# Kernel optimization log

Hardware: AMD Instinct MI355X
Metric: run time of the kernel (lower is better)

## Reference

```python
import jax, jax.numpy as jnp
import numpy as np

CODE_DIM = 256
CODEBOOK_SIZE = 8192
N = 32768
BETA = 0.25


def setup_inputs() -> dict:
    key = jax.random.key(0)
    k1, k2 = jax.random.split(key)
    z = jax.random.normal(k1, (N, CODE_DIM), dtype=jnp.float32)
    # nn.Embedding weight init: uniform(-1/code_dim, 1/code_dim)
    codebook = jax.random.uniform(
        k2, (CODEBOOK_SIZE, CODE_DIM), dtype=jnp.float32,
        minval=-1.0 / CODE_DIM, maxval=1.0 / CODE_DIM)
    return {"z": z, "codebook": codebook}


def reference(z, codebook):
    # z: (N, D) already flat (z.view(N, -1) in torch). codebook: (K, D)
    # squared euclidean distances via expansion: ||z||^2 - 2 z.E^T + ||E||^2
    z_sq = jnp.sum(z * z, axis=1, keepdims=True)            # (N, 1)
    e_sq = jnp.sum(codebook * codebook, axis=1)             # (K,)
    dist = z_sq - 2.0 * (z @ codebook.T) + e_sq[None, :]    # (N, K)
    indices = jnp.argmin(dist, axis=1)                      # (N,)
    z_q = codebook[indices]                                 # (N, D)

    commitment_loss = jnp.mean((jax.lax.stop_gradient(z_q) - z) ** 2)
    codebook_loss = jnp.mean((z_q - jax.lax.stop_gradient(z)) ** 2)
    loss = BETA * commitment_loss + codebook_loss

    # straight-through estimator
    z_q_ste = z + jax.lax.stop_gradient(z_q - z)
    return (z_q_ste, loss)
```

## Files before the change

### kernel.cpp

```cpp
#include <hip/hip_runtime.h>
#include <cfloat>

#define NROWS  32768
#define NCODES 8192
#define DDIM   256
#define KG     4
#define CPB    (NCODES / KG)
#define CT     64
#define TPB    (CPB / CT)
#define RPB    256

typedef __attribute__((ext_vector_type(8))) __bf16 bf16x8;
typedef __attribute__((ext_vector_type(4))) float  f32x4;

__global__ __launch_bounds__(256)
void cvt_cb(const float* __restrict__ cb, __bf16* __restrict__ cbb,
            float* __restrict__ esq) {
    const size_t i = (size_t)(blockIdx.x * 256 + threadIdx.x) * 8;
    const float4 f0 = *(const float4*)(cb + i);
    const float4 f1 = *(const float4*)(cb + i + 4);
    bf16x8 v;
    v[0] = (__bf16)f0.x; v[1] = (__bf16)f0.y; v[2] = (__bf16)f0.z; v[3] = (__bf16)f0.w;
    v[4] = (__bf16)f1.x; v[5] = (__bf16)f1.y; v[6] = (__bf16)f1.z; v[7] = (__bf16)f1.w;
    *(bf16x8*)(cbb + i) = v;
    float s = f0.x * f0.x + f0.y * f0.y + f0.z * f0.z + f0.w * f0.w
            + f1.x * f1.x + f1.y * f1.y + f1.z * f1.z + f1.w * f1.w;
    for (int o = 16; o > 0; o >>= 1) s += __shfl_down(s, o, 32);
    if ((threadIdx.x & 31) == 0) esq[i >> 8] = s;
}

__global__ __launch_bounds__(256, 2)
void vq_mfma(const float* __restrict__ z, const __bf16* __restrict__ cbb,
             const float* __restrict__ esq,
             float* __restrict__ pV, int* __restrict__ pI) {
    __shared__ __align__(16) __bf16 Bb[2][CT * DDIM];

    const int rowbase  = (blockIdx.x >> 2) * RPB;
    const int kg       = blockIdx.x & 3;
    const int codebase = kg * CPB;

    const int tid = threadIdx.x;
    const int w = tid >> 6, l = tid & 63;
    const int lm = l & 15, lq = l >> 4;
    const int loff = lm * DDIM + lq * 8;

#pragma unroll
    for (int j = 0; j < 8; ++j) {
        __builtin_amdgcn_global_load_lds(
            (const __attribute__((address_space(1))) void*)
                (cbb + (size_t)(codebase + w * 16) * DDIM + j * 32 + loff),
            (__attribute__((address_space(3))) void*)(&Bb[0][(j * 4 + w) * 512]),
            16, 0, 0);
    }

    bf16x8 Af[4][8];
    {
        const float* zp = z + (size_t)(rowbase + w * 64 + lm) * DDIM + lq * 8;
#pragma unroll
        for (int s = 0; s < 4; ++s)
#pragma unroll
            for (int kc = 0; kc < 8; ++kc) {
                const float4 f0 = *(const float4*)(zp + s * 16 * DDIM + kc * 32);
                const float4 f1 = *(const float4*)(zp + s * 16 * DDIM + kc * 32 + 4);
                bf16x8 v;
                v[0] = (__bf16)(-2.f * f0.x); v[1] = (__bf16)(-2.f * f0.y);
                v[2] = (__bf16)(-2.f * f0.z); v[3] = (__bf16)(-2.f * f0.w);
                v[4] = (__bf16)(-2.f * f1.x); v[5] = (__bf16)(-2.f * f1.y);
                v[6] = (__bf16)(-2.f * f1.z); v[7] = (__bf16)(-2.f * f1.w);
                Af[s][kc] = v;
            }
    }

    float evc[4], evn[4];
#pragma unroll
    for (int fc = 0; fc < 4; ++fc)
        evc[fc] = esq[codebase + fc * 16 + lm];

    float bestV[16];
    int   bestI[16];
#pragma unroll
    for (int s = 0; s < 16; ++s) { bestV[s] = FLT_MAX; bestI[s] = 0; }

    __syncthreads();

    int buf = 0;
#pragma unroll 1
    for (int t = 0; t < TPB; ++t) {
        if (t + 1 < TPB) {
            const __bf16* base = cbb + (size_t)(codebase + (t + 1) * CT + w * 16) * DDIM;
#pragma unroll
            for (int j = 0; j < 8; ++j) {
                __builtin_amdgcn_global_load_lds(
                    (const __attribute__((address_space(1))) void*)(base + j * 32 + loff),
                    (__attribute__((address_space(3))) void*)(&Bb[buf ^ 1][(j * 4 + w) * 512]),
                    16, 0, 0);
            }
        }
        {
            const int tn = (t + 1) & (TPB - 1);
#pragma unroll
            for (int fc = 0; fc < 4; ++fc)
                evn[fc] = esq[codebase + tn * CT + fc * 16 + lm];
        }

        const __bf16* Bc = &Bb[buf][0];
#pragma unroll
        for (int fch = 0; fch < 2; ++fch) {
            f32x4 acc[4][2];
#pragma unroll
            for (int fr = 0; fr < 4; ++fr)
#pragma unroll
                for (int fc = 0; fc < 2; ++fc) {
                    const float e = evc[fch * 2 + fc];
                    acc[fr][fc] = (f32x4){e, e, e, e};
                }

#pragma unroll
            for (int c = 0; c < 8; ++c) {
                const bf16x8 b0 = *(const bf16x8*)(Bc + (c * 4 + fch * 2 + 0) * 512 + l * 8);
                const bf16x8 b1 = *(const bf16x8*)(Bc + (c * 4 + fch * 2 + 1) * 512 + l * 8);
#pragma unroll
                for (int fr = 0; fr < 4; ++fr)
                    acc[fr][0] = __builtin_amdgcn_mfma_f32_16x16x32_bf16(
                        Af[fr][c], b0, acc[fr][0], 0, 0, 0);
#pragma unroll
                for (int fr = 0; fr < 4; ++fr)
                    acc[fr][1] = __builtin_amdgcn_mfma_f32_16x16x32_bf16(
                        Af[fr][c], b1, acc[fr][1], 0, 0, 0);
            }

#pragma unroll
            for (int fr = 0; fr < 4; ++fr)
#pragma unroll
                for (int fc = 0; fc < 2; ++fc) {
                    const int colI = codebase + t * CT + (fch * 2 + fc) * 16 + lm;
#pragma unroll
                    for (int i = 0; i < 4; ++i) {
                        const float sc = acc[fr][fc][i];
                        const int slot = fr * 4 + i;
                        if (sc < bestV[slot]) { bestV[slot] = sc; bestI[slot] = colI; }
                    }
                }
        }
#pragma unroll
        for (int fc = 0; fc < 4; ++fc) evc[fc] = evn[fc];

        __syncthreads();
        buf ^= 1;
    }

#pragma unroll
    for (int s = 0; s < 16; ++s) {
#pragma unroll
        for (int m = 1; m < 16; m <<= 1) {
            const float v2 = __shfl_xor(bestV[s], m);
            const int   i2 = __shfl_xor(bestI[s], m);
            if (v2 < bestV[s] || (v2 == bestV[s] && i2 < bestI[s])) {
                bestV[s] = v2; bestI[s] = i2;
            }
        }
    }
    if (lm == 0) {
#pragma unroll
        for (int s = 0; s < 16; ++s) {
            const int rl = w * 64 + (s >> 2) * 16 + lq * 4 + (s & 3);
            const int row = rowbase + rl;
            pV[row * KG + kg] = bestV[s];
            pI[row * KG + kg] = bestI[s];
        }
    }
}

__global__ __launch_bounds__(256)
void vq_finalize(const float* __restrict__ z, const float* __restrict__ cb,
                 const float* __restrict__ pV, const int* __restrict__ pI,
                 float* __restrict__ out, float* __restrict__ bsum) {
    __shared__ float sSum[4];
    __shared__ int   sIdx[4];
    const int tid = threadIdx.x;
    const int rw = tid >> 6, lane = tid & 63;
    const int row = blockIdx.x * 4 + rw;

    if (lane == 0) {
        float v = pV[row * KG]; int bi = pI[row * KG];
#pragma unroll
        for (int q = 1; q < KG; ++q) {
            const float v2 = pV[row * KG + q]; const int i2 = pI[row * KG + q];
            if (v2 < v || (v2 == v && i2 < bi)) { v = v2; bi = i2; }
        }
        sIdx[rw] = bi;
    }
    __syncthreads();
    const int idx = sIdx[rw];

    const float4 zv = *(const float4*)(z  + (size_t)row * DDIM + lane * 4);
    const float4 ev = *(const float4*)(cb + (size_t)idx * DDIM + lane * 4);
    float4 d, o;
    d.x = ev.x - zv.x; d.y = ev.y - zv.y; d.z = ev.z - zv.z; d.w = ev.w - zv.w;
    o.x = zv.x + d.x;  o.y = zv.y + d.y;  o.z = zv.z + d.z;  o.w = zv.w + d.w;
    *(float4*)(out + (size_t)row * DDIM + lane * 4) = o;

    float s = d.x * d.x + d.y * d.y + d.z * d.z + d.w * d.w;
    for (int off = 32; off > 0; off >>= 1) s += __shfl_down(s, off);
    if (lane == 0) sSum[rw] = s;
    __syncthreads();
    if (tid == 0) bsum[blockIdx.x] = sSum[0] + sSum[1] + sSum[2] + sSum[3];
}

__global__ __launch_bounds__(256)
void loss_final(const float* __restrict__ bsum, float* __restrict__ out) {
    __shared__ float red[4];
    const int tid = threadIdx.x;
    float s = 0.f;
    for (int i = tid; i < NROWS / 4; i += 256) s += bsum[i];
    for (int off = 32; off > 0; off >>= 1) s += __shfl_down(s, off);
    const int wv = tid >> 6, lane = tid & 63;
    if (lane == 0) red[wv] = s;
    __syncthreads();
    if (tid == 0) {
        const float tot = red[0] + red[1] + red[2] + red[3];
        out[(size_t)NROWS * DDIM] = tot * (1.25f / (float)((size_t)NROWS * DDIM));
    }
}

extern "C" void kernel_launch(void* const* d_in, const int* in_sizes, int n_in,
                              void* d_out, int out_size, void* d_ws, size_t ws_size,
                              hipStream_t stream) {
    const float* z  = (const float*)d_in[0];
    const float* cb = (const float*)d_in[1];
    float* out = (float*)d_out;

    __bf16* cbf = (__bf16*)d_out;

    float* esq  = (float*)d_ws;
    float* pV   = esq + NCODES;
    int*   pI   = (int*)(pV + NROWS * KG);
    float* bsum = (float*)(pI + NROWS * KG);

    cvt_cb<<<NCODES * DDIM / 8 / 256, 256, 0, stream>>>(cb, cbf, esq);
    vq_mfma<<<(NROWS / RPB) * KG, 256, 0, stream>>>(z, cbf, esq, pV, pI);
    vq_finalize<<<NROWS / 4, 256, 0, stream>>>(z, cb, pV, pI, out, bsum);
    loss_final<<<1, 256, 0, stream>>>(bsum, out);
}
```

Before: 246.8 us.

## Pack distance and index into one sortable key and software-pipeline argmin

Adds 1.0 to each codebook norm so that every distance stays positive, which lets the float bits compare correctly as unsigned integers. The low 13 mantissa bits are then replaced with the code index, so the argmin becomes a single unsigned min per element. The argmin epilogue of one half-tile is moved so it runs while the MFMAs of the other half are issued, hiding compare latency behind matrix work. The cost is lower distance precision, since 13 mantissa bits are dropped and ties resolve by index, and more live accumulator registers (two sets of accumulators).

```diff
diff --git a/kernel.cpp b/kernel.cpp
--- a/kernel.cpp
+++ b/kernel.cpp
@@ -26,13 +26,12 @@
     float s = f0.x * f0.x + f0.y * f0.y + f0.z * f0.z + f0.w * f0.w
             + f1.x * f1.x + f1.y * f1.y + f1.z * f1.z + f1.w * f1.w;
     for (int o = 16; o > 0; o >>= 1) s += __shfl_down(s, o, 32);
-    if ((threadIdx.x & 31) == 0) esq[i >> 8] = s;
+    if ((threadIdx.x & 31) == 0) esq[i >> 8] = s + 1.0f;
 }
 
 __global__ __launch_bounds__(256, 2)
 void vq_mfma(const float* __restrict__ z, const __bf16* __restrict__ cbb,
-             const float* __restrict__ esq,
-             float* __restrict__ pV, int* __restrict__ pI) {
+             const float* __restrict__ esq, unsigned* __restrict__ pK) {
     __shared__ __align__(16) __bf16 Bb[2][CT * DDIM];
 
     const int rowbase  = (blockIdx.x >> 2) * RPB;
@@ -76,10 +75,17 @@
     for (int fc = 0; fc < 4; ++fc)
         evc[fc] = esq[codebase + fc * 16 + lm];
 
-    float bestV[16];
-    int   bestI[16];
-#pragma unroll
-    for (int s = 0; s < 16; ++s) { bestV[s] = FLT_MAX; bestI[s] = 0; }
+    unsigned bestK[16];
+#pragma unroll
+    for (int s = 0; s < 16; ++s) bestK[s] = 0xFFFFFFFFu;
+
+    f32x4 accB[4][2];
+#pragma unroll
+    for (int fr = 0; fr < 4; ++fr) {
+        accB[fr][0] = (f32x4){2.f, 2.f, 2.f, 2.f};
+        accB[fr][1] = (f32x4){2.f, 2.f, 2.f, 2.f};
+    }
+    int pB = codebase;
 
     __syncthreads();
 
@@ -104,44 +110,80 @@
         }
 
         const __bf16* Bc = &Bb[buf][0];
-#pragma unroll
-        for (int fch = 0; fch < 2; ++fch) {
-            f32x4 acc[4][2];
-#pragma unroll
-            for (int fr = 0; fr < 4; ++fr)
-#pragma unroll
-                for (int fc = 0; fc < 2; ++fc) {
-                    const float e = evc[fch * 2 + fc];
-                    acc[fr][fc] = (f32x4){e, e, e, e};
+
+        f32x4 accA[4][2];
+#pragma unroll
+        for (int fr = 0; fr < 4; ++fr) {
+            const float e0 = evc[0], e1 = evc[1];
+            accA[fr][0] = (f32x4){e0, e0, e0, e0};
+            accA[fr][1] = (f32x4){e1, e1, e1, e1};
+        }
+#pragma unroll
+        for (int c = 0; c < 8; ++c) {
+            const bf16x8 b0 = *(const bf16x8*)(Bc + (c * 4 + 0) * 512 + l * 8);
+            const bf16x8 b1 = *(const bf16x8*)(Bc + (c * 4 + 1) * 512 + l * 8);
+#pragma unroll
+            for (int fr = 0; fr < 4; ++fr)
+                accA[fr][0] = __builtin_amdgcn_mfma_f32_16x16x32_bf16(
+                    Af[fr][c], b0, accA[fr][0], 0, 0, 0);
+#pragma unroll
+            for (int fr = 0; fr < 4; ++fr)
+                accA[fr][1] = __builtin_amdgcn_mfma_f32_16x16x32_bf16(
+                    Af[fr][c], b1, accA[fr][1], 0, 0, 0);
+        }
+
+        {
+            const unsigned c0 = (unsigned)(pB + lm);
+            const unsigned c1 = (unsigned)(pB + 16 + lm);
+#pragma unroll
+            for (int fr = 0; fr < 4; ++fr)
+#pragma unroll
+                for (int i = 0; i < 4; ++i) {
+                    const int slot = fr * 4 + i;
+                    const unsigned k0 = (__float_as_uint(accB[fr][0][i]) & 0xFFFFE000u) | c0;
+                    const unsigned k1 = (__float_as_uint(accB[fr][1][i]) & 0xFFFFE000u) | c1;
+                    const unsigned km = k0 < k1 ? k0 : k1;
+                    if (km < bestK[slot]) bestK[slot] = km;
                 }
-
-#pragma unroll
-            for (int c = 0; c < 8; ++c) {
-                const bf16x8 b0 = *(const bf16x8*)(Bc + (c * 4 + fch * 2 + 0) * 512 + l * 8);
-                const bf16x8 b1 = *(const bf16x8*)(Bc + (c * 4 + fch * 2 + 1) * 512 + l * 8);
-#pragma unroll
-                for (int fr = 0; fr < 4; ++fr)
-                    acc[fr][0] = __builtin_amdgcn_mfma_f32_16x16x32_bf16(
-                        Af[fr][c], b0, acc[fr][0], 0, 0, 0);
-#pragma unroll
-                for (int fr = 0; fr < 4; ++fr)
-                    acc[fr][1] = __builtin_amdgcn_mfma_f32_16x16x32_bf16(
-                        Af[fr][c], b1, acc[fr][1], 0, 0, 0);
-            }
-
-#pragma unroll
-            for (int fr = 0; fr < 4; ++fr)
-#pragma unroll
-                for (int fc = 0; fc < 2; ++fc) {
-                    const int colI = codebase + t * CT + (fch * 2 + fc) * 16 + lm;
-#pragma unroll
-                    for (int i = 0; i < 4; ++i) {
-                        const float sc = acc[fr][fc][i];
-                        const int slot = fr * 4 + i;
-                        if (sc < bestV[slot]) { bestV[slot] = sc; bestI[slot] = colI; }
-                    }
+        }
+
+#pragma unroll
+        for (int fr = 0; fr < 4; ++fr) {
+            const float e2 = evc[2], e3 = evc[3];
+            accB[fr][0] = (f32x4){e2, e2, e2, e2};
+            accB[fr][1] = (f32x4){e3, e3, e3, e3};
+        }
+#pragma unroll
+        for (int c = 0; c < 8; ++c) {
+            const bf16x8 b2 = *(const bf16x8*)(Bc + (c * 4 + 2) * 512 + l * 8);
+            const bf16x8 b3 = *(const bf16x8*)(Bc + (c * 4 + 3) * 512 + l * 8);
+#pragma unroll
+            for (int fr = 0; fr < 4; ++fr)
+                accB[fr][0] = __builtin_amdgcn_mfma_f32_16x16x32_bf16(
+                    Af[fr][c], b2, accB[fr][0], 0, 0, 0);
+#pragma unroll
+            for (int fr = 0; fr < 4; ++fr)
+                accB[fr][1] = __builtin_amdgcn_mfma_f32_16x16x32_bf16(
+                    Af[fr][c], b3, accB[fr][1], 0, 0, 0);
+        }
+
+        {
+            const int base0 = codebase + t * CT;
+            const unsigned c0 = (unsigned)(base0 + lm);
+            const unsigned c1 = (unsigned)(base0 + 16 + lm);
+#pragma unroll
+            for (int fr = 0; fr < 4; ++fr)
+#pragma unroll
+                for (int i = 0; i < 4; ++i) {
+                    const int slot = fr * 4 + i;
+                    const unsigned k0 = (__float_as_uint(accA[fr][0][i]) & 0xFFFFE000u) | c0;
+                    const unsigned k1 = (__float_as_uint(accA[fr][1][i]) & 0xFFFFE000u) | c1;
+                    const unsigned km = k0 < k1 ? k0 : k1;
+                    if (km < bestK[slot]) bestK[slot] = km;
                 }
         }
+        pB = codebase + t * CT + 32;
+
 #pragma unroll
         for (int fc = 0; fc < 4; ++fc) evc[fc] = evn[fc];
 
@@ -149,15 +191,27 @@
         buf ^= 1;
     }
 
+    {
+        const unsigned c0 = (unsigned)(pB + lm);
+        const unsigned c1 = (unsigned)(pB + 16 + lm);
+#pragma unroll
+        for (int fr = 0; fr < 4; ++fr)
+#pragma unroll
+            for (int i = 0; i < 4; ++i) {
+                const int slot = fr * 4 + i;
+                const unsigned k0 = (__float_as_uint(accB[fr][0][i]) & 0xFFFFE000u) | c0;
+                const unsigned k1 = (__float_as_uint(accB[fr][1][i]) & 0xFFFFE000u) | c1;
+                const unsigned km = k0 < k1 ? k0 : k1;
+                if (km < bestK[slot]) bestK[slot] = km;
+            }
+    }
+
 #pragma unroll
     for (int s = 0; s < 16; ++s) {
 #pragma unroll
         for (int m = 1; m < 16; m <<= 1) {
-            const float v2 = __shfl_xor(bestV[s], m);
-            const int   i2 = __shfl_xor(bestI[s], m);
-            if (v2 < bestV[s] || (v2 == bestV[s] && i2 < bestI[s])) {
-                bestV[s] = v2; bestI[s] = i2;
-            }
+            const unsigned k2 = (unsigned)__shfl_xor((int)bestK[s], m);
+            if (k2 < bestK[s]) bestK[s] = k2;
         }
     }
     if (lm == 0) {
@@ -165,15 +219,14 @@
         for (int s = 0; s < 16; ++s) {
             const int rl = w * 64 + (s >> 2) * 16 + lq * 4 + (s & 3);
             const int row = rowbase + rl;
-            pV[row * KG + kg] = bestV[s];
-            pI[row * KG + kg] = bestI[s];
+            pK[row * KG + kg] = bestK[s];
         }
     }
 }
 
 __global__ __launch_bounds__(256)
 void vq_finalize(const float* __restrict__ z, const float* __restrict__ cb,
-                 const float* __restrict__ pV, const int* __restrict__ pI,
+                 const unsigned* __restrict__ pK,
                  float* __restrict__ out, float* __restrict__ bsum) {
     __shared__ float sSum[4];
     __shared__ int   sIdx[4];
@@ -182,13 +235,13 @@
     const int row = blockIdx.x * 4 + rw;
 
     if (lane == 0) {
-        float v = pV[row * KG]; int bi = pI[row * KG];
+        unsigned k = pK[row * KG];
 #pragma unroll
         for (int q = 1; q < KG; ++q) {
-            const float v2 = pV[row * KG + q]; const int i2 = pI[row * KG + q];
-            if (v2 < v || (v2 == v && i2 < bi)) { v = v2; bi = i2; }
-        }
-        sIdx[rw] = bi;
+            const unsigned k2 = pK[row * KG + q];
+            if (k2 < k) k = k2;
+        }
+        sIdx[rw] = (int)(k & 0x1FFFu);
     }
     __syncthreads();
     const int idx = sIdx[rw];
@@ -232,13 +285,12 @@
 
     __bf16* cbf = (__bf16*)d_out;
 
-    float* esq  = (float*)d_ws;
-    float* pV   = esq + NCODES;
-    int*   pI   = (int*)(pV + NROWS * KG);
-    float* bsum = (float*)(pI + NROWS * KG);
+    float*    esq  = (float*)d_ws;
+    unsigned* pK   = (unsigned*)(esq + NCODES);
+    float*    bsum = (float*)(pK + NROWS * KG);
 
     cvt_cb<<<NCODES * DDIM / 8 / 256, 256, 0, stream>>>(cb, cbf, esq);
-    vq_mfma<<<(NROWS / RPB) * KG, 256, 0, stream>>>(z, cbf, esq, pV, pI);
-    vq_finalize<<<NROWS / 4, 256, 0, stream>>>(z, cb, pV, pI, out, bsum);
+    vq_mfma<<<(NROWS / RPB) * KG, 256, 0, stream>>>(z, cbf, esq, pK);
+    vq_finalize<<<NROWS / 4, 256, 0, stream>>>(z, cb, pK, out, bsum);
     loss_final<<<1, 256, 0, stream>>>(bsum, out);
 }
```

After: 228.8 us. 1.08x faster.

## Switch to 32x32x16 MFMA with packed value-index argmin keys and software pipelining

Applied to the files above, without the earlier changes.

Replaces the 16x16x32 bf16 MFMA tiling with 32x32x16 tiles, reorganising the LDS codebook layout and A-fragment registers to match. The argmin now packs the truncated distance bits and a 13-bit code index into a single unsigned key, offset by +1 so distances stay positive, which turns the compare-and-select into one unsigned min and simplifies the cross-lane and cross-group reductions. The argmin of one half-tile is deferred so it overlaps with the MFMAs of the next half-tile. The key packing drops the low mantissa bits, so near-ties may resolve differently from the reference.

```diff
diff --git a/kernel.cpp b/kernel.cpp
--- a/kernel.cpp
+++ b/kernel.cpp
@@ -10,8 +10,8 @@
 #define TPB    (CPB / CT)
 #define RPB    256
 
-typedef __attribute__((ext_vector_type(8))) __bf16 bf16x8;
-typedef __attribute__((ext_vector_type(4))) float  f32x4;
+typedef __attribute__((ext_vector_type(8)))  __bf16 bf16x8;
+typedef __attribute__((ext_vector_type(16))) float  f32x16;
 
 __global__ __launch_bounds__(256)
 void cvt_cb(const float* __restrict__ cb, __bf16* __restrict__ cbb,
@@ -26,13 +26,12 @@
     float s = f0.x * f0.x + f0.y * f0.y + f0.z * f0.z + f0.w * f0.w
             + f1.x * f1.x + f1.y * f1.y + f1.z * f1.z + f1.w * f1.w;
     for (int o = 16; o > 0; o >>= 1) s += __shfl_down(s, o, 32);
-    if ((threadIdx.x & 31) == 0) esq[i >> 8] = s;
+    if ((threadIdx.x & 31) == 0) esq[i >> 8] = s + 1.0f;
 }
 
 __global__ __launch_bounds__(256, 2)
 void vq_mfma(const float* __restrict__ z, const __bf16* __restrict__ cbb,
-             const float* __restrict__ esq,
-             float* __restrict__ pV, int* __restrict__ pI) {
+             const float* __restrict__ esq, unsigned* __restrict__ pK) {
     __shared__ __align__(16) __bf16 Bb[2][CT * DDIM];
 
     const int rowbase  = (blockIdx.x >> 2) * RPB;
@@ -41,27 +40,29 @@
 
     const int tid = threadIdx.x;
     const int w = tid >> 6, l = tid & 63;
-    const int lm = l & 15, lq = l >> 4;
-    const int loff = lm * DDIM + lq * 8;
-
-#pragma unroll
-    for (int j = 0; j < 8; ++j) {
+    const int la = l & 31, lh = l >> 5;
+    const int loff = la * DDIM + lh * 8;
+
+#pragma unroll
+    for (int jj = 0; jj < 8; ++jj) {
+        const int p = w * 8 + jj;
+        const int fc = p >> 4, kc = p & 15;
         __builtin_amdgcn_global_load_lds(
             (const __attribute__((address_space(1))) void*)
-                (cbb + (size_t)(codebase + w * 16) * DDIM + j * 32 + loff),
-            (__attribute__((address_space(3))) void*)(&Bb[0][(j * 4 + w) * 512]),
+                (cbb + (size_t)(codebase + fc * 32) * DDIM + kc * 16 + loff),
+            (__attribute__((address_space(3))) void*)(&Bb[0][p * 512]),
             16, 0, 0);
     }
 
-    bf16x8 Af[4][8];
+    bf16x8 Af[2][16];
     {
-        const float* zp = z + (size_t)(rowbase + w * 64 + lm) * DDIM + lq * 8;
-#pragma unroll
-        for (int s = 0; s < 4; ++s)
-#pragma unroll
-            for (int kc = 0; kc < 8; ++kc) {
-                const float4 f0 = *(const float4*)(zp + s * 16 * DDIM + kc * 32);
-                const float4 f1 = *(const float4*)(zp + s * 16 * DDIM + kc * 32 + 4);
+        const float* zp = z + (size_t)(rowbase + w * 64 + la) * DDIM + lh * 8;
+#pragma unroll
+        for (int s = 0; s < 2; ++s)
+#pragma unroll
+            for (int kc = 0; kc < 16; ++kc) {
+                const float4 f0 = *(const float4*)(zp + s * 32 * DDIM + kc * 16);
+                const float4 f1 = *(const float4*)(zp + s * 32 * DDIM + kc * 16 + 4);
                 bf16x8 v;
                 v[0] = (__bf16)(-2.f * f0.x); v[1] = (__bf16)(-2.f * f0.y);
                 v[2] = (__bf16)(-2.f * f0.z); v[3] = (__bf16)(-2.f * f0.w);
@@ -71,15 +72,18 @@
             }
     }
 
-    float evc[4], evn[4];
-#pragma unroll
-    for (int fc = 0; fc < 4; ++fc)
-        evc[fc] = esq[codebase + fc * 16 + lm];
-
-    float bestV[16];
-    int   bestI[16];
-#pragma unroll
-    for (int s = 0; s < 16; ++s) { bestV[s] = FLT_MAX; bestI[s] = 0; }
+    float evc[2], evn[2];
+    evc[0] = esq[codebase + la];
+    evc[1] = esq[codebase + 32 + la];
+
+    unsigned bestK[32];
+#pragma unroll
+    for (int s = 0; s < 32; ++s) bestK[s] = 0xFFFFFFFFu;
+
+    f32x16 accB0, accB1;
+#pragma unroll
+    for (int r = 0; r < 16; ++r) { accB0[r] = 2.f; accB1[r] = 2.f; }
+    int pB = codebase;
 
     __syncthreads();
 
@@ -87,93 +91,107 @@
 #pragma unroll 1
     for (int t = 0; t < TPB; ++t) {
         if (t + 1 < TPB) {
-            const __bf16* base = cbb + (size_t)(codebase + (t + 1) * CT + w * 16) * DDIM;
-#pragma unroll
-            for (int j = 0; j < 8; ++j) {
+            const __bf16* base = cbb + (size_t)(codebase + (t + 1) * CT) * DDIM;
+#pragma unroll
+            for (int jj = 0; jj < 8; ++jj) {
+                const int p = w * 8 + jj;
+                const int fc = p >> 4, kc = p & 15;
                 __builtin_amdgcn_global_load_lds(
-                    (const __attribute__((address_space(1))) void*)(base + j * 32 + loff),
-                    (__attribute__((address_space(3))) void*)(&Bb[buf ^ 1][(j * 4 + w) * 512]),
+                    (const __attribute__((address_space(1))) void*)
+                        (base + (size_t)(fc * 32) * DDIM + kc * 16 + loff),
+                    (__attribute__((address_space(3))) void*)(&Bb[buf ^ 1][p * 512]),
                     16, 0, 0);
             }
         }
         {
             const int tn = (t + 1) & (TPB - 1);
-#pragma unroll
-            for (int fc = 0; fc < 4; ++fc)
-                evn[fc] = esq[codebase + tn * CT + fc * 16 + lm];
+            evn[0] = esq[codebase + tn * CT + la];
+            evn[1] = esq[codebase + tn * CT + 32 + la];
         }
 
         const __bf16* Bc = &Bb[buf][0];
-#pragma unroll
-        for (int fch = 0; fch < 2; ++fch) {
-            f32x4 acc[4][2];
-#pragma unroll
-            for (int fr = 0; fr < 4; ++fr)
-#pragma unroll
-                for (int fc = 0; fc < 2; ++fc) {
-                    const float e = evc[fch * 2 + fc];
-                    acc[fr][fc] = (f32x4){e, e, e, e};
-                }
-
-#pragma unroll
-            for (int c = 0; c < 8; ++c) {
-                const bf16x8 b0 = *(const bf16x8*)(Bc + (c * 4 + fch * 2 + 0) * 512 + l * 8);
-                const bf16x8 b1 = *(const bf16x8*)(Bc + (c * 4 + fch * 2 + 1) * 512 + l * 8);
-#pragma unroll
-                for (int fr = 0; fr < 4; ++fr)
-                    acc[fr][0] = __builtin_amdgcn_mfma_f32_16x16x32_bf16(
-                        Af[fr][c], b0, acc[fr][0], 0, 0, 0);
-#pragma unroll
-                for (int fr = 0; fr < 4; ++fr)
-                    acc[fr][1] = __builtin_amdgcn_mfma_f32_16x16x32_bf16(
-                        Af[fr][c], b1, acc[fr][1], 0, 0, 0);
-            }
-
-#pragma unroll
-            for (int fr = 0; fr < 4; ++fr)
-#pragma unroll
-                for (int fc = 0; fc < 2; ++fc) {
-                    const int colI = codebase + t * CT + (fch * 2 + fc) * 16 + lm;
-#pragma unroll
-                    for (int i = 0; i < 4; ++i) {
-                        const float sc = acc[fr][fc][i];
-                        const int slot = fr * 4 + i;
-                        if (sc < bestV[slot]) { bestV[slot] = sc; bestI[slot] = colI; }
-                    }
-                }
-        }
-#pragma unroll
-        for (int fc = 0; fc < 4; ++fc) evc[fc] = evn[fc];
+
+        f32x16 accA0, accA1;
+#pragma unroll
+        for (int r = 0; r < 16; ++r) { accA0[r] = evc[0]; accA1[r] = evc[0]; }
+#pragma unroll
+        for (int kc = 0; kc < 16; ++kc) {
+            const bf16x8 b = *(const bf16x8*)(Bc + kc * 512 + l * 8);
+            accA0 = __builtin_amdgcn_mfma_f32_32x32x16_bf16(Af[0][kc], b, accA0, 0, 0, 0);
+            accA1 = __builtin_amdgcn_mfma_f32_32x32x16_bf16(Af[1][kc], b, accA1, 0, 0, 0);
+        }
+
+        {
+            const unsigned cB = (unsigned)(pB + la);
+#pragma unroll
+            for (int r = 0; r < 16; ++r) {
+                const unsigned k0 = (__float_as_uint(accB0[r]) & 0xFFFFE000u) | cB;
+                if (k0 < bestK[r])      bestK[r]      = k0;
+                const unsigned k1 = (__float_as_uint(accB1[r]) & 0xFFFFE000u) | cB;
+                if (k1 < bestK[16 + r]) bestK[16 + r] = k1;
+            }
+        }
+
+#pragma unroll
+        for (int r = 0; r < 16; ++r) { accB0[r] = evc[1]; accB1[r] = evc[1]; }
+#pragma unroll
+        for (int kc = 0; kc < 16; ++kc) {
+            const bf16x8 b = *(const bf16x8*)(Bc + (16 + kc) * 512 + l * 8);
+            accB0 = __builtin_amdgcn_mfma_f32_32x32x16_bf16(Af[0][kc], b, accB0, 0, 0, 0);
+            accB1 = __builtin_amdgcn_mfma_f32_32x32x16_bf16(Af[1][kc], b, accB1, 0, 0, 0);
+        }
+
+        {
+            const unsigned cA = (unsigned)(codebase + t * CT + la);
+#pragma unroll
+            for (int r = 0; r < 16; ++r) {
+                const unsigned k0 = (__float_as_uint(accA0[r]) & 0xFFFFE000u) | cA;
+                if (k0 < bestK[r])      bestK[r]      = k0;
+                const unsigned k1 = (__float_as_uint(accA1[r]) & 0xFFFFE000u) | cA;
+                if (k1 < bestK[16 + r]) bestK[16 + r] = k1;
+            }
+        }
+        pB = codebase + t * CT + 32;
+
+        evc[0] = evn[0]; evc[1] = evn[1];
 
         __syncthreads();
         buf ^= 1;
     }
 
-#pragma unroll
-    for (int s = 0; s < 16; ++s) {
-#pragma unroll
-        for (int m = 1; m < 16; m <<= 1) {
-            const float v2 = __shfl_xor(bestV[s], m);
-            const int   i2 = __shfl_xor(bestI[s], m);
-            if (v2 < bestV[s] || (v2 == bestV[s] && i2 < bestI[s])) {
-                bestV[s] = v2; bestI[s] = i2;
-            }
-        }
-    }
-    if (lm == 0) {
-#pragma unroll
-        for (int s = 0; s < 16; ++s) {
-            const int rl = w * 64 + (s >> 2) * 16 + lq * 4 + (s & 3);
-            const int row = rowbase + rl;
-            pV[row * KG + kg] = bestV[s];
-            pI[row * KG + kg] = bestI[s];
-        }
+    {
+        const unsigned cB = (unsigned)(pB + la);
+#pragma unroll
+        for (int r = 0; r < 16; ++r) {
+            const unsigned k0 = (__float_as_uint(accB0[r]) & 0xFFFFE000u) | cB;
+            if (k0 < bestK[r])      bestK[r]      = k0;
+            const unsigned k1 = (__float_as_uint(accB1[r]) & 0xFFFFE000u) | cB;
+            if (k1 < bestK[16 + r]) bestK[16 + r] = k1;
+        }
+    }
+
+#pragma unroll
+    for (int s = 0; s < 32; ++s) {
+#pragma unroll
+        for (int m = 1; m < 32; m <<= 1) {
+            const unsigned k2 = (unsigned)__shfl_xor((int)bestK[s], m);
+            if (k2 < bestK[s]) bestK[s] = k2;
+        }
+    }
+    if (la == 0) {
+#pragma unroll
+        for (int s = 0; s < 2; ++s)
+#pragma unroll
+            for (int r = 0; r < 16; ++r) {
+                const int rl = w * 64 + s * 32 + (r & 3) + 8 * (r >> 2) + 4 * lh;
+                pK[(size_t)(rowbase + rl) * KG + kg] = bestK[s * 16 + r];
+            }
     }
 }
 
 __global__ __launch_bounds__(256)
 void vq_finalize(const float* __restrict__ z, const float* __restrict__ cb,
-                 const float* __restrict__ pV, const int* __restrict__ pI,
+                 const unsigned* __restrict__ pK,
                  float* __restrict__ out, float* __restrict__ bsum) {
     __shared__ float sSum[4];
     __shared__ int   sIdx[4];
@@ -182,13 +200,13 @@
     const int row = blockIdx.x * 4 + rw;
 
     if (lane == 0) {
-        float v = pV[row * KG]; int bi = pI[row * KG];
+        unsigned k = pK[row * KG];
 #pragma unroll
         for (int q = 1; q < KG; ++q) {
-            const float v2 = pV[row * KG + q]; const int i2 = pI[row * KG + q];
-            if (v2 < v || (v2 == v && i2 < bi)) { v = v2; bi = i2; }
-        }
-        sIdx[rw] = bi;
+            const unsigned k2 = pK[row * KG + q];
+            if (k2 < k) k = k2;
+        }
+        sIdx[rw] = (int)(k & 0x1FFFu);
     }
     __syncthreads();
     const int idx = sIdx[rw];
@@ -232,13 +250,12 @@
 
     __bf16* cbf = (__bf16*)d_out;
 
-    float* esq  = (float*)d_ws;
-    float* pV   = esq + NCODES;
-    int*   pI   = (int*)(pV + NROWS * KG);
-    float* bsum = (float*)(pI + NROWS * KG);
+    float*    esq  = (float*)d_ws;
+    unsigned* pK   = (unsigned*)(esq + NCODES);
+    float*    bsum = (float*)(pK + NROWS * KG);
 
     cvt_cb<<<NCODES * DDIM / 8 / 256, 256, 0, stream>>>(cb, cbf, esq);
-    vq_mfma<<<(NROWS / RPB) * KG, 256, 0, stream>>>(z, cbf, esq, pV, pI);
-    vq_finalize<<<NROWS / 4, 256, 0, stream>>>(z, cb, pV, pI, out, bsum);
+    vq_mfma<<<(NROWS / RPB) * KG, 256, 0, stream>>>(z, cbf, esq, pK);
+    vq_finalize<<<NROWS / 4, 256, 0, stream>>>(z, cb, pK, out, bsum);
     loss_final<<<1, 256, 0, stream>>>(bsum, out);
 }
```

New measurement: 293.8 us. 1.19x slower.
